# Optimization experiments

Hardware: AMD Instinct MI355X
Metric: run time of the kernel (lower is better)

Reference implementation:

```python
import jax, jax.numpy as jnp
import numpy as np

N, VQ, VK, C, H = 4, 4096, 4096, 128, 64


def setup_inputs() -> dict:
    key = jax.random.key(0)
    kx, ky, kq, kk, kv = jax.random.split(key, 5)
    # xavier-uniform-ish scale for params
    def xavier(k, shape):
        fan_in, fan_out = shape
        lim = (6.0 / (fan_in + fan_out)) ** 0.5
        return jax.random.uniform(k, shape, jnp.float32, -lim, lim)
    return {
        "x": jax.random.normal(kx, (N, VQ, C), jnp.float32),
        "y": jax.random.normal(ky, (N, VK, C), jnp.float32),
        "Wq": xavier(kq, (C, H)),
        "Wk": xavier(kk, (C, H)),
        "Wv": xavier(kv, (C, C)),
    }


def reference(x, y, Wq, Wk, Wv):
    # x: [n, vq, c], y: [n, vk, c]
    scale = Wq.shape[1] ** (-0.5)
    q = jnp.einsum('nvc,co->nvo', x, Wq)   # [n, vq, h]
    k = jnp.einsum('nvc,co->nvo', y, Wk)   # [n, vk, h]
    v = jnp.einsum('nvc,co->nvo', y, Wv)   # [n, vk, c]
    scores = jnp.einsum('nqc,nkc->nqk', q, k) * scale  # [n, vq, vk]
    attn = jax.nn.softmax(scores, axis=-1)
    return jnp.einsum('nqk,nkc->nqc', attn, v)         # [n, vq, c]
```

## Files before the change

kernel.cpp:

```cpp
#include <hip/hip_runtime.h>

typedef __bf16 bf16x8 __attribute__((ext_vector_type(8)));
typedef __bf16 bf16x4 __attribute__((ext_vector_type(4)));
typedef __bf16 bf16x2 __attribute__((ext_vector_type(2)));
typedef float  f32x4  __attribute__((ext_vector_type(4)));
typedef float  f32x16 __attribute__((ext_vector_type(16)));
typedef int    i32x4  __attribute__((ext_vector_type(4)));

#define MFMA16 __builtin_amdgcn_mfma_f32_16x16x32_bf16
#define MFMA32 __builtin_amdgcn_mfma_f32_32x32x16_bf16

static constexpr int BATCH = 4;
static constexpr int SEQ   = 4096;
static constexpr int CDIM  = 128;
static constexpr int HDIM  = 64;
static constexpr float FIXMAX = 16.0f;

union FB2  { bf16x2 h; int i; };
union I4B8 { i32x4 i; bf16x8 b; };

__device__ inline bf16x8 load8f_cvt(const float* __restrict__ p) {
    f32x4 a = *reinterpret_cast<const f32x4*>(p);
    f32x4 b = *reinterpret_cast<const f32x4*>(p + 4);
    bf16x8 r;
    r[0] = (__bf16)a[0]; r[1] = (__bf16)a[1]; r[2] = (__bf16)a[2]; r[3] = (__bf16)a[3];
    r[4] = (__bf16)b[0]; r[5] = (__bf16)b[1]; r[6] = (__bf16)b[2]; r[7] = (__bf16)b[3];
    return r;
}


__global__ __launch_bounds__(256) void proj_all_kernel(
    const float* __restrict__ x, const float* __restrict__ y,
    const float* __restrict__ Wq, const float* __restrict__ Wk,
    const float* __restrict__ Wv,
    __bf16* __restrict__ Qw, __bf16* __restrict__ Kw, __bf16* __restrict__ Vtw,
    float qscale)
{
    __shared__ __bf16 Wt[64][136];
    __shared__ __bf16 Vtile[64][72];

    const int job = blockIdx.x >> 8;
    const int bx  = blockIdx.x & 255;
    const int t    = threadIdx.x;
    const int lane = t & 63;
    const int w    = t >> 6;
    const int m    = lane & 15;
    const int quad = lane >> 4;

    if (job <= 1) {
        const float* X    = job ? y  : x;
        const float* W    = job ? Wk : Wq;
        __bf16*      outp = job ? Kw : Qw;
        const float scale = job ? 1.0f : qscale;

        #pragma unroll
        for (int pass = 0; pass < 4; ++pass) {
            int flat = pass * 2048 + t * 8;
            int cin  = flat >> 6;
            int h0   = flat & 63;
            bf16x8 v = load8f_cvt(W + flat);
            #pragma unroll
            for (int j = 0; j < 8; ++j) Wt[h0 + j][cin] = v[j];
        }
        __syncthreads();

        const int row0 = bx * 64 + w * 16;
        bf16x8 af[4];
        #pragma unroll
        for (int kc = 0; kc < 4; ++kc)
            af[kc] = load8f_cvt(X + (long)(row0 + m) * 128 + kc * 32 + quad * 8);

        #pragma unroll
        for (int tn = 0; tn < 4; ++tn) {
            f32x4 acc = {0.f, 0.f, 0.f, 0.f};
            #pragma unroll
            for (int kc = 0; kc < 4; ++kc) {
                bf16x8 bfrag = *reinterpret_cast<const bf16x8*>(&Wt[tn * 16 + m][kc * 32 + quad * 8]);
                acc = MFMA16(af[kc], bfrag, acc, 0, 0, 0);
            }
            #pragma unroll
            for (int r = 0; r < 4; ++r) {
                int  kg   = row0 + quad * 4 + r;
                long addr = ((long)(kg >> 5) * 4 + tn) * 512
                          + ((m >> 3) * 32 + (kg & 31)) * 8 + (m & 7);
                outp[addr] = (__bf16)(acc[r] * scale);
            }
        }
    } else {
        const int cob = (job - 2) * 64;
        const int ct0 = (job - 2) * 2;

        #pragma unroll
        for (int pass = 0; pass < 4; ++pass) {
            int flat = pass * 2048 + t * 8;
            int cin  = flat >> 6;
            int co0  = flat & 63;
            bf16x8 v = load8f_cvt(Wv + cin * 128 + cob + co0);
            #pragma unroll
            for (int j = 0; j < 8; ++j) Wt[co0 + j][cin] = v[j];
        }
        __syncthreads();

        const int row0 = bx * 64 + w * 16;
        bf16x8 af[4];
        #pragma unroll
        for (int kc = 0; kc < 4; ++kc)
            af[kc] = load8f_cvt(y + (long)(row0 + m) * 128 + kc * 32 + quad * 8);

        #pragma unroll
        for (int tn = 0; tn < 4; ++tn) {
            f32x4 acc = {0.f, 0.f, 0.f, 0.f};
            #pragma unroll
            for (int kc = 0; kc < 4; ++kc) {
                bf16x8 bfrag = *reinterpret_cast<const bf16x8*>(&Wt[tn * 16 + m][kc * 32 + quad * 8]);
                acc = MFMA16(af[kc], bfrag, acc, 0, 0, 0);
            }
            bf16x4 pk;
            #pragma unroll
            for (int r = 0; r < 4; ++r) pk[r] = (__bf16)acc[r];
            *reinterpret_cast<bf16x4*>(&Vtile[tn * 16 + m][w * 16 + quad * 4]) = pk;
        }
        __syncthreads();

        #pragma unroll
        for (int pp = 0; pp < 2; ++pp) {
            int i       = pp * 256 + t;
            int c_local = i & 31;
            int hh      = (i >> 5) & 1;
            int kc2     = (i >> 6) & 1;
            int ct_l    = (i >> 7) & 1;
            int kt_l    = i >> 8;
            bf16x8 v = *reinterpret_cast<const bf16x8*>(
                &Vtile[ct_l * 32 + c_local][kt_l * 32 + kc2 * 16 + hh * 8]);
            long dst = ((long)(bx * 2 + kt_l) * 8 + (ct0 + ct_l) * 2 + kc2) * 512
                     + (hh * 32 + c_local) * 8;
            *reinterpret_cast<bf16x8*>(Vtw + dst) = v;
        }
    }
}

__device__ __forceinline__ void attn_iter(
    const bf16x8 (&qf)[4],
    const bf16x8 (&kf)[4], bf16x8 (&kfn)[4],
    const bf16x8 (&vf)[8], bf16x8 (&vfn)[8],
    const __bf16* __restrict__ kp_next, const __bf16* __restrict__ vp_next,
    bool prefetch, f32x16 (&o_acc)[4],
    float& l_a, float& l_b, float& l_c, float& l_d)
{
    if (prefetch) {
        #pragma unroll
        for (int kc = 0; kc < 4; ++kc)
            kfn[kc] = *reinterpret_cast<const bf16x8*>(kp_next + kc * 512);
        #pragma unroll
        for (int c = 0; c < 8; ++c)
            vfn[c] = *reinterpret_cast<const bf16x8*>(vp_next + c * 512);
    }

    f32x16 s;
    #pragma unroll
    for (int i = 0; i < 16; ++i) s[i] = -FIXMAX;
    __builtin_amdgcn_s_setprio(1);
    #pragma unroll
    for (int kc = 0; kc < 4; ++kc)
        s = MFMA32(kf[kc], qf[kc], s, 0, 0, 0);
    __builtin_amdgcn_s_setprio(0);

    #pragma unroll
    for (int kc2 = 0; kc2 < 2; ++kc2) {
        float& lx = kc2 ? l_c : l_a;
        float& ly = kc2 ? l_d : l_b;
        int Dw[4];
        #pragma unroll
        for (int r2 = 0; r2 < 4; ++r2) {
            float p0 = __builtin_amdgcn_exp2f(s[8 * kc2 + 2 * r2]);
            float p1 = __builtin_amdgcn_exp2f(s[8 * kc2 + 2 * r2 + 1]);
            lx += p0; ly += p1;
            FB2 u; u.h[0] = (__bf16)p0; u.h[1] = (__bf16)p1;
            Dw[r2] = u.i;
        }
        int a0 = Dw[0], a1 = Dw[1], a2 = Dw[2], a3 = Dw[3];
        asm("v_permlane32_swap_b32 %0, %1" : "+v"(a0), "+v"(a2));
        asm("v_permlane32_swap_b32 %0, %1" : "+v"(a1), "+v"(a3));
        I4B8 pb;
        pb.i[0] = a0;
        pb.i[1] = a1;
        pb.i[2] = a2;
        pb.i[3] = a3;
        __builtin_amdgcn_s_setprio(1);
        #pragma unroll
        for (int ct = 0; ct < 4; ++ct)
            o_acc[ct] = MFMA32(vf[ct * 2 + kc2], pb.b, o_acc[ct], 0, 0, 0);
        __builtin_amdgcn_s_setprio(0);
    }
}

__global__ __launch_bounds__(512, 2) void attn_kernel(
    const __bf16* __restrict__ Qs, const __bf16* __restrict__ Ks,
    const __bf16* __restrict__ Vs, float* __restrict__ out)
{
    __shared__ float mbuf[2][2][64][65];

    const int t    = threadIdx.x;
    const int lane = t & 63;
    const int w    = t >> 6;
    const int qs   = w & 1;
    const int g    = w >> 1;
    const int qc   = lane & 31;
    const int h    = lane >> 5;

    const int bx  = blockIdx.x;
    const int n   = bx >> 6;
    const int qtl = bx & 63;

    const long QT = (long)n * 128 + qtl * 2 + qs;
    bf16x8 qf[4];
    #pragma unroll
    for (int kc = 0; kc < 4; ++kc)
        qf[kc] = *reinterpret_cast<const bf16x8*>(Qs + (QT * 4 + kc) * 512 + lane * 8);

    const __bf16* kb = Ks + ((long)n * 128 + g * 32) * 2048 + lane * 8;
    const __bf16* vb = Vs + ((long)n * 128 + g * 32) * 4096 + lane * 8;

    f32x16 o_acc[4];
    #pragma unroll
    for (int a = 0; a < 4; ++a)
        #pragma unroll
        for (int i = 0; i < 16; ++i) o_acc[a][i] = 0.f;
    float l_a = 0.f, l_b = 0.f, l_c = 0.f, l_d = 0.f;

    bf16x8 kf0[4], kf1[4];
    bf16x8 vf0[8], vf1[8];

    #pragma unroll
    for (int kc = 0; kc < 4; ++kc)
        kf0[kc] = *reinterpret_cast<const bf16x8*>(kb + kc * 512);
    #pragma unroll
    for (int c = 0; c < 8; ++c)
        vf0[c] = *reinterpret_cast<const bf16x8*>(vb + c * 512);

    for (int kt = 0; kt < 32; kt += 2) {
        attn_iter(qf, kf0, kf1, vf0, vf1,
                  kb + (long)(kt + 1) * 2048, vb + (long)(kt + 1) * 4096,
                  true, o_acc, l_a, l_b, l_c, l_d);
        attn_iter(qf, kf1, kf0, vf1, vf0,
                  kb + (long)(kt + 2) * 2048, vb + (long)(kt + 2) * 4096,
                  kt < 30, o_acc, l_a, l_b, l_c, l_d);
    }

    float l_run = (l_a + l_b) + (l_c + l_d);

    if (g >= 2) {
        float* dst = &mbuf[qs][g - 2][lane][0];
        #pragma unroll
        for (int ct = 0; ct < 4; ++ct)
            #pragma unroll
            for (int i = 0; i < 16; ++i) dst[ct * 16 + i] = o_acc[ct][i];
        dst[64] = l_run;
    }
    __syncthreads();
    if (g < 2) {
        const float* src = &mbuf[qs][g][lane][0];
        #pragma unroll
        for (int ct = 0; ct < 4; ++ct)
            #pragma unroll
            for (int i = 0; i < 16; ++i) o_acc[ct][i] += src[ct * 16 + i];
        l_run += src[64];
    }
    __syncthreads();
    if (g == 1) {
        float* dst = &mbuf[qs][0][lane][0];
        #pragma unroll
        for (int ct = 0; ct < 4; ++ct)
            #pragma unroll
            for (int i = 0; i < 16; ++i) dst[ct * 16 + i] = o_acc[ct][i];
        dst[64] = l_run;
    }
    __syncthreads();

    if (g == 0) {
        const float* src = &mbuf[qs][0][lane][0];
        #pragma unroll
        for (int ct = 0; ct < 4; ++ct)
            #pragma unroll
            for (int i = 0; i < 16; ++i) o_acc[ct][i] += src[ct * 16 + i];
        l_run += src[64];

        l_run += __shfl_xor(l_run, 32, 64);
        const float inv = 1.0f / l_run;
        const long row = (long)n * SEQ + qtl * 64 + qs * 32 + qc;
        #pragma unroll
        for (int ct = 0; ct < 4; ++ct)
            #pragma unroll
            for (int rg = 0; rg < 4; ++rg) {
                f32x4 o;
                #pragma unroll
                for (int i = 0; i < 4; ++i) o[i] = o_acc[ct][rg * 4 + i] * inv;
                *reinterpret_cast<f32x4*>(
                    out + row * CDIM + ct * 32 + rg * 8 + h * 4) = o;
            }
    }
}

extern "C" void kernel_launch(void* const* d_in, const int* in_sizes, int n_in,
                              void* d_out, int out_size, void* d_ws, size_t ws_size,
                              hipStream_t stream)
{
    const float* x  = (const float*)d_in[0];
    const float* y  = (const float*)d_in[1];
    const float* Wq = (const float*)d_in[2];
    const float* Wk = (const float*)d_in[3];
    const float* Wv = (const float*)d_in[4];
    float* out = (float*)d_out;

    __bf16* Qw  = (__bf16*)d_ws;
    __bf16* Kw  = Qw + (long)BATCH * SEQ * HDIM;
    __bf16* Vtw = Kw + (long)BATCH * SEQ * HDIM;

    const float qscale = 0.125f * 1.4426950408889634f;

    proj_all_kernel<<<dim3(1024), dim3(256), 0, stream>>>(
        x, y, Wq, Wk, Wv, Qw, Kw, Vtw, qscale);

    attn_kernel<<<dim3(256), dim3(512), 0, stream>>>(Qw, Kw, Vtw, out);
}
```

Baseline: 110.0 us.

## Split attention output channels across wave pairs and double the grid

Result: slower. 120.1 us (+9.2%).

```diff
diff --git a/kernel.cpp b/kernel.cpp
--- a/kernel.cpp
+++ b/kernel.cpp
@@ -139,164 +139,136 @@
     }
 }
 
-__device__ __forceinline__ void attn_iter(
-    const bf16x8 (&qf)[4],
-    const bf16x8 (&kf)[4], bf16x8 (&kfn)[4],
-    const bf16x8 (&vf)[8], bf16x8 (&vfn)[8],
-    const __bf16* __restrict__ kp_next, const __bf16* __restrict__ vp_next,
-    bool prefetch, f32x16 (&o_acc)[4],
-    float& l_a, float& l_b, float& l_c, float& l_d)
-{
-    if (prefetch) {
-        #pragma unroll
-        for (int kc = 0; kc < 4; ++kc)
-            kfn[kc] = *reinterpret_cast<const bf16x8*>(kp_next + kc * 512);
-        #pragma unroll
-        for (int c = 0; c < 8; ++c)
-            vfn[c] = *reinterpret_cast<const bf16x8*>(vp_next + c * 512);
-    }
-
-    f32x16 s;
-    #pragma unroll
-    for (int i = 0; i < 16; ++i) s[i] = -FIXMAX;
-    __builtin_amdgcn_s_setprio(1);
-    #pragma unroll
-    for (int kc = 0; kc < 4; ++kc)
-        s = MFMA32(kf[kc], qf[kc], s, 0, 0, 0);
-    __builtin_amdgcn_s_setprio(0);
-
-    #pragma unroll
-    for (int kc2 = 0; kc2 < 2; ++kc2) {
-        float& lx = kc2 ? l_c : l_a;
-        float& ly = kc2 ? l_d : l_b;
-        int Dw[4];
-        #pragma unroll
-        for (int r2 = 0; r2 < 4; ++r2) {
-            float p0 = __builtin_amdgcn_exp2f(s[8 * kc2 + 2 * r2]);
-            float p1 = __builtin_amdgcn_exp2f(s[8 * kc2 + 2 * r2 + 1]);
-            lx += p0; ly += p1;
-            FB2 u; u.h[0] = (__bf16)p0; u.h[1] = (__bf16)p1;
-            Dw[r2] = u.i;
-        }
-        int a0 = Dw[0], a1 = Dw[1], a2 = Dw[2], a3 = Dw[3];
-        asm("v_permlane32_swap_b32 %0, %1" : "+v"(a0), "+v"(a2));
-        asm("v_permlane32_swap_b32 %0, %1" : "+v"(a1), "+v"(a3));
-        I4B8 pb;
-        pb.i[0] = a0;
-        pb.i[1] = a1;
-        pb.i[2] = a2;
-        pb.i[3] = a3;
-        __builtin_amdgcn_s_setprio(1);
-        #pragma unroll
-        for (int ct = 0; ct < 4; ++ct)
-            o_acc[ct] = MFMA32(vf[ct * 2 + kc2], pb.b, o_acc[ct], 0, 0, 0);
-        __builtin_amdgcn_s_setprio(0);
-    }
-}
-
-__global__ __launch_bounds__(512, 2) void attn_kernel(
+__global__ __launch_bounds__(512, 4) void attn_kernel(
     const __bf16* __restrict__ Qs, const __bf16* __restrict__ Ks,
     const __bf16* __restrict__ Vs, float* __restrict__ out)
 {
-    __shared__ float mbuf[2][2][64][65];
+    __shared__ float mbuf[2][2][64][33];
 
     const int t    = threadIdx.x;
     const int lane = t & 63;
     const int w    = t >> 6;
-    const int qs   = w & 1;
+    const int ch   = w & 1;
     const int g    = w >> 1;
     const int qc   = lane & 31;
     const int h    = lane >> 5;
 
-    const int bx  = blockIdx.x;
-    const int n   = bx >> 6;
-    const int qtl = bx & 63;
-
-    const long QT = (long)n * 128 + qtl * 2 + qs;
+    const int bx   = blockIdx.x;
+    const int n    = bx >> 7;
+    const int qsub = bx & 127;
+
+    const long QT = (long)n * 128 + qsub;
     bf16x8 qf[4];
     #pragma unroll
     for (int kc = 0; kc < 4; ++kc)
         qf[kc] = *reinterpret_cast<const bf16x8*>(Qs + (QT * 4 + kc) * 512 + lane * 8);
 
     const __bf16* kb = Ks + ((long)n * 128 + g * 32) * 2048 + lane * 8;
-    const __bf16* vb = Vs + ((long)n * 128 + g * 32) * 4096 + lane * 8;
-
-    f32x16 o_acc[4];
+    const __bf16* vb = Vs + ((long)n * 128 + g * 32) * 4096 + ch * 2048 + lane * 8;
+
+    f32x16 o_acc[2];
     #pragma unroll
-    for (int a = 0; a < 4; ++a)
+    for (int a = 0; a < 2; ++a)
         #pragma unroll
         for (int i = 0; i < 16; ++i) o_acc[a][i] = 0.f;
     float l_a = 0.f, l_b = 0.f, l_c = 0.f, l_d = 0.f;
 
-    bf16x8 kf0[4], kf1[4];
-    bf16x8 vf0[8], vf1[8];
-
-    #pragma unroll
-    for (int kc = 0; kc < 4; ++kc)
-        kf0[kc] = *reinterpret_cast<const bf16x8*>(kb + kc * 512);
-    #pragma unroll
-    for (int c = 0; c < 8; ++c)
-        vf0[c] = *reinterpret_cast<const bf16x8*>(vb + c * 512);
-
-    for (int kt = 0; kt < 32; kt += 2) {
-        attn_iter(qf, kf0, kf1, vf0, vf1,
-                  kb + (long)(kt + 1) * 2048, vb + (long)(kt + 1) * 4096,
-                  true, o_acc, l_a, l_b, l_c, l_d);
-        attn_iter(qf, kf1, kf0, vf1, vf0,
-                  kb + (long)(kt + 2) * 2048, vb + (long)(kt + 2) * 4096,
-                  kt < 30, o_acc, l_a, l_b, l_c, l_d);
+    for (int kt = 0; kt < 32; ++kt) {
+        bf16x8 kf[4], vf[4];
+        #pragma unroll
+        for (int kc = 0; kc < 4; ++kc)
+            kf[kc] = *reinterpret_cast<const bf16x8*>(kb + ((long)kt * 4 + kc) * 512);
+        #pragma unroll
+        for (int c = 0; c < 4; ++c)
+            vf[c] = *reinterpret_cast<const bf16x8*>(vb + (long)kt * 4096 + c * 512);
+
+        f32x16 s;
+        #pragma unroll
+        for (int i = 0; i < 16; ++i) s[i] = -FIXMAX;
+        __builtin_amdgcn_s_setprio(1);
+        #pragma unroll
+        for (int kc = 0; kc < 4; ++kc)
+            s = MFMA32(kf[kc], qf[kc], s, 0, 0, 0);
+        __builtin_amdgcn_s_setprio(0);
+
+        #pragma unroll
+        for (int kc2 = 0; kc2 < 2; ++kc2) {
+            float& lx = kc2 ? l_c : l_a;
+            float& ly = kc2 ? l_d : l_b;
+            int Dw[4];
+            #pragma unroll
+            for (int r2 = 0; r2 < 4; ++r2) {
+                float p0 = __builtin_amdgcn_exp2f(s[8 * kc2 + 2 * r2]);
+                float p1 = __builtin_amdgcn_exp2f(s[8 * kc2 + 2 * r2 + 1]);
+                lx += p0; ly += p1;
+                FB2 u; u.h[0] = (__bf16)p0; u.h[1] = (__bf16)p1;
+                Dw[r2] = u.i;
+            }
+            int a0 = Dw[0], a1 = Dw[1], a2 = Dw[2], a3 = Dw[3];
+            asm("v_permlane32_swap_b32 %0, %1" : "+v"(a0), "+v"(a2));
+            asm("v_permlane32_swap_b32 %0, %1" : "+v"(a1), "+v"(a3));
+            I4B8 pb;
+            pb.i[0] = a0;
+            pb.i[1] = a1;
+            pb.i[2] = a2;
+            pb.i[3] = a3;
+            __builtin_amdgcn_s_setprio(1);
+            o_acc[0] = MFMA32(vf[kc2],     pb.b, o_acc[0], 0, 0, 0);
+            o_acc[1] = MFMA32(vf[2 + kc2], pb.b, o_acc[1], 0, 0, 0);
+            __builtin_amdgcn_s_setprio(0);
+        }
     }
 
     float l_run = (l_a + l_b) + (l_c + l_d);
 
     if (g >= 2) {
-        float* dst = &mbuf[qs][g - 2][lane][0];
-        #pragma unroll
-        for (int ct = 0; ct < 4; ++ct)
-            #pragma unroll
-            for (int i = 0; i < 16; ++i) dst[ct * 16 + i] = o_acc[ct][i];
-        dst[64] = l_run;
+        float* dst = &mbuf[ch][g - 2][lane][0];
+        #pragma unroll
+        for (int ctl = 0; ctl < 2; ++ctl)
+            #pragma unroll
+            for (int i = 0; i < 16; ++i) dst[ctl * 16 + i] = o_acc[ctl][i];
+        dst[32] = l_run;
     }
     __syncthreads();
     if (g < 2) {
-        const float* src = &mbuf[qs][g][lane][0];
-        #pragma unroll
-        for (int ct = 0; ct < 4; ++ct)
-            #pragma unroll
-            for (int i = 0; i < 16; ++i) o_acc[ct][i] += src[ct * 16 + i];
-        l_run += src[64];
+        const float* src = &mbuf[ch][g][lane][0];
+        #pragma unroll
+        for (int ctl = 0; ctl < 2; ++ctl)
+            #pragma unroll
+            for (int i = 0; i < 16; ++i) o_acc[ctl][i] += src[ctl * 16 + i];
+        l_run += src[32];
     }
     __syncthreads();
     if (g == 1) {
-        float* dst = &mbuf[qs][0][lane][0];
-        #pragma unroll
-        for (int ct = 0; ct < 4; ++ct)
-            #pragma unroll
-            for (int i = 0; i < 16; ++i) dst[ct * 16 + i] = o_acc[ct][i];
-        dst[64] = l_run;
+        float* dst = &mbuf[ch][0][lane][0];
+        #pragma unroll
+        for (int ctl = 0; ctl < 2; ++ctl)
+            #pragma unroll
+            for (int i = 0; i < 16; ++i) dst[ctl * 16 + i] = o_acc[ctl][i];
+        dst[32] = l_run;
     }
     __syncthreads();
 
     if (g == 0) {
-        const float* src = &mbuf[qs][0][lane][0];
-        #pragma unroll
-        for (int ct = 0; ct < 4; ++ct)
-            #pragma unroll
-            for (int i = 0; i < 16; ++i) o_acc[ct][i] += src[ct * 16 + i];
-        l_run += src[64];
+        const float* src = &mbuf[ch][0][lane][0];
+        #pragma unroll
+        for (int ctl = 0; ctl < 2; ++ctl)
+            #pragma unroll
+            for (int i = 0; i < 16; ++i) o_acc[ctl][i] += src[ctl * 16 + i];
+        l_run += src[32];
 
         l_run += __shfl_xor(l_run, 32, 64);
         const float inv = 1.0f / l_run;
-        const long row = (long)n * SEQ + qtl * 64 + qs * 32 + qc;
-        #pragma unroll
-        for (int ct = 0; ct < 4; ++ct)
+        const long row = (long)n * SEQ + qsub * 32 + qc;
+        #pragma unroll
+        for (int ctl = 0; ctl < 2; ++ctl)
             #pragma unroll
             for (int rg = 0; rg < 4; ++rg) {
                 f32x4 o;
                 #pragma unroll
-                for (int i = 0; i < 4; ++i) o[i] = o_acc[ct][rg * 4 + i] * inv;
+                for (int i = 0; i < 4; ++i) o[i] = o_acc[ctl][rg * 4 + i] * inv;
                 *reinterpret_cast<f32x4*>(
-                    out + row * CDIM + ct * 32 + rg * 8 + h * 4) = o;
+                    out + row * CDIM + ch * 64 + ctl * 32 + rg * 8 + h * 4) = o;
             }
     }
 }
@@ -321,5 +293,5 @@
     proj_all_kernel<<<dim3(1024), dim3(256), 0, stream>>>(
         x, y, Wq, Wk, Wv, Qw, Kw, Vtw, qscale);
 
-    attn_kernel<<<dim3(256), dim3(512), 0, stream>>>(Qw, Kw, Vtw, out);
-}
+    attn_kernel<<<dim3(512), dim3(512), 0, stream>>>(Qw, Kw, Vtw, out);
+}
```

## Split attention blocks to one query tile and drop V double-buffering

Applied to the files above, without the earlier changes.

New measurement: 177.5 us. 1.61x slower.

```diff
diff --git a/kernel.cpp b/kernel.cpp
--- a/kernel.cpp
+++ b/kernel.cpp
@@ -142,18 +142,18 @@
 __device__ __forceinline__ void attn_iter(
     const bf16x8 (&qf)[4],
     const bf16x8 (&kf)[4], bf16x8 (&kfn)[4],
-    const bf16x8 (&vf)[8], bf16x8 (&vfn)[8],
-    const __bf16* __restrict__ kp_next, const __bf16* __restrict__ vp_next,
-    bool prefetch, f32x16 (&o_acc)[4],
-    float& l_a, float& l_b, float& l_c, float& l_d)
+    const __bf16* __restrict__ vp,
+    const __bf16* __restrict__ kp_next,
+    bool prefetch, f32x16 (&o_acc)[4], float& l_a, float& l_b)
 {
+    bf16x8 vfA[4];
+    #pragma unroll
+    for (int ct = 0; ct < 4; ++ct)
+        vfA[ct] = *reinterpret_cast<const bf16x8*>(vp + (2 * ct) * 512);
     if (prefetch) {
         #pragma unroll
         for (int kc = 0; kc < 4; ++kc)
             kfn[kc] = *reinterpret_cast<const bf16x8*>(kp_next + kc * 512);
-        #pragma unroll
-        for (int c = 0; c < 8; ++c)
-            vfn[c] = *reinterpret_cast<const bf16x8*>(vp_next + c * 512);
     }
 
     f32x16 s;
@@ -165,16 +165,19 @@
         s = MFMA32(kf[kc], qf[kc], s, 0, 0, 0);
     __builtin_amdgcn_s_setprio(0);
 
+    bf16x8 vfB[4];
+    #pragma unroll
+    for (int ct = 0; ct < 4; ++ct)
+        vfB[ct] = *reinterpret_cast<const bf16x8*>(vp + (2 * ct + 1) * 512);
+
     #pragma unroll
     for (int kc2 = 0; kc2 < 2; ++kc2) {
-        float& lx = kc2 ? l_c : l_a;
-        float& ly = kc2 ? l_d : l_b;
         int Dw[4];
         #pragma unroll
         for (int r2 = 0; r2 < 4; ++r2) {
             float p0 = __builtin_amdgcn_exp2f(s[8 * kc2 + 2 * r2]);
             float p1 = __builtin_amdgcn_exp2f(s[8 * kc2 + 2 * r2 + 1]);
-            lx += p0; ly += p1;
+            l_a += p0; l_b += p1;
             FB2 u; u.h[0] = (__bf16)p0; u.h[1] = (__bf16)p1;
             Dw[r2] = u.i;
         }
@@ -189,30 +192,28 @@
         __builtin_amdgcn_s_setprio(1);
         #pragma unroll
         for (int ct = 0; ct < 4; ++ct)
-            o_acc[ct] = MFMA32(vf[ct * 2 + kc2], pb.b, o_acc[ct], 0, 0, 0);
+            o_acc[ct] = MFMA32(kc2 ? vfB[ct] : vfA[ct], pb.b, o_acc[ct], 0, 0, 0);
         __builtin_amdgcn_s_setprio(0);
     }
 }
 
-__global__ __launch_bounds__(512, 2) void attn_kernel(
+__global__ __launch_bounds__(256, 3) void attn_kernel(
     const __bf16* __restrict__ Qs, const __bf16* __restrict__ Ks,
     const __bf16* __restrict__ Vs, float* __restrict__ out)
 {
-    __shared__ float mbuf[2][2][64][65];
+    __shared__ float mbuf[2][64][65];
 
     const int t    = threadIdx.x;
     const int lane = t & 63;
-    const int w    = t >> 6;
-    const int qs   = w & 1;
-    const int g    = w >> 1;
+    const int g    = t >> 6;
     const int qc   = lane & 31;
     const int h    = lane >> 5;
 
-    const int bx  = blockIdx.x;
-    const int n   = bx >> 6;
-    const int qtl = bx & 63;
-
-    const long QT = (long)n * 128 + qtl * 2 + qs;
+    const int bx   = blockIdx.x;
+    const int n    = bx >> 7;
+    const int qsub = bx & 127;
+
+    const long QT = (long)n * 128 + qsub;
     bf16x8 qf[4];
     #pragma unroll
     for (int kc = 0; kc < 4; ++kc)
@@ -226,31 +227,27 @@
     for (int a = 0; a < 4; ++a)
         #pragma unroll
         for (int i = 0; i < 16; ++i) o_acc[a][i] = 0.f;
-    float l_a = 0.f, l_b = 0.f, l_c = 0.f, l_d = 0.f;
+    float l_a = 0.f, l_b = 0.f;
 
     bf16x8 kf0[4], kf1[4];
-    bf16x8 vf0[8], vf1[8];
 
     #pragma unroll
     for (int kc = 0; kc < 4; ++kc)
         kf0[kc] = *reinterpret_cast<const bf16x8*>(kb + kc * 512);
-    #pragma unroll
-    for (int c = 0; c < 8; ++c)
-        vf0[c] = *reinterpret_cast<const bf16x8*>(vb + c * 512);
 
     for (int kt = 0; kt < 32; kt += 2) {
-        attn_iter(qf, kf0, kf1, vf0, vf1,
-                  kb + (long)(kt + 1) * 2048, vb + (long)(kt + 1) * 4096,
-                  true, o_acc, l_a, l_b, l_c, l_d);
-        attn_iter(qf, kf1, kf0, vf1, vf0,
-                  kb + (long)(kt + 2) * 2048, vb + (long)(kt + 2) * 4096,
-                  kt < 30, o_acc, l_a, l_b, l_c, l_d);
-    }
-
-    float l_run = (l_a + l_b) + (l_c + l_d);
+        attn_iter(qf, kf0, kf1, vb + (long)kt * 4096,
+                  kb + (long)(kt + 1) * 2048,
+                  true, o_acc, l_a, l_b);
+        attn_iter(qf, kf1, kf0, vb + (long)(kt + 1) * 4096,
+                  kb + (long)(kt + 2) * 2048,
+                  kt < 30, o_acc, l_a, l_b);
+    }
+
+    float l_run = l_a + l_b;
 
     if (g >= 2) {
-        float* dst = &mbuf[qs][g - 2][lane][0];
+        float* dst = &mbuf[g - 2][lane][0];
         #pragma unroll
         for (int ct = 0; ct < 4; ++ct)
             #pragma unroll
@@ -259,7 +256,7 @@
     }
     __syncthreads();
     if (g < 2) {
-        const float* src = &mbuf[qs][g][lane][0];
+        const float* src = &mbuf[g][lane][0];
         #pragma unroll
         for (int ct = 0; ct < 4; ++ct)
             #pragma unroll
@@ -268,7 +265,7 @@
     }
     __syncthreads();
     if (g == 1) {
-        float* dst = &mbuf[qs][0][lane][0];
+        float* dst = &mbuf[0][lane][0];
         #pragma unroll
         for (int ct = 0; ct < 4; ++ct)
             #pragma unroll
@@ -278,7 +275,7 @@
     __syncthreads();
 
     if (g == 0) {
-        const float* src = &mbuf[qs][0][lane][0];
+        const float* src = &mbuf[0][lane][0];
         #pragma unroll
         for (int ct = 0; ct < 4; ++ct)
             #pragma unroll
@@ -287,7 +284,7 @@
 
         l_run += __shfl_xor(l_run, 32, 64);
         const float inv = 1.0f / l_run;
-        const long row = (long)n * SEQ + qtl * 64 + qs * 32 + qc;
+        const long row = (long)n * SEQ + qsub * 32 + qc;
         #pragma unroll
         for (int ct = 0; ct < 4; ++ct)
             #pragma unroll
@@ -321,5 +318,5 @@
     proj_all_kernel<<<dim3(1024), dim3(256), 0, stream>>>(
         x, y, Wq, Wk, Wv, Qw, Kw, Vtw, qscale);
 
-    attn_kernel<<<dim3(256), dim3(512), 0, stream>>>(Qw, Kw, Vtw, out);
-}
+    attn_kernel<<<dim3(512), dim3(256), 0, stream>>>(Qw, Kw, Vtw, out);
+}
```

## Software-pipeline QK^T one tile ahead of softmax and PV in attention loop

Applied to the files above, without the earlier changes.

Measured after the change: 110.2 us. About the same (+0.2%).

```diff
diff --git a/kernel.cpp b/kernel.cpp
--- a/kernel.cpp
+++ b/kernel.cpp
@@ -141,29 +141,36 @@
 
 __device__ __forceinline__ void attn_iter(
     const bf16x8 (&qf)[4],
-    const bf16x8 (&kf)[4], bf16x8 (&kfn)[4],
-    const bf16x8 (&vf)[8], bf16x8 (&vfn)[8],
-    const __bf16* __restrict__ kp_next, const __bf16* __restrict__ vp_next,
-    bool prefetch, f32x16 (&o_acc)[4],
+    const bf16x8 (&kfq)[4],
+    bf16x8 (&kfp)[4],
+    const bf16x8 (&vf)[8],
+    bf16x8 (&vfp)[8],
+    const __bf16* __restrict__ kp2, const __bf16* __restrict__ vp1,
+    bool pref_k, bool pref_v, bool do_qk,
+    f32x16& s_cur, f32x16& s_next,
+    f32x16 (&o_acc)[4],
     float& l_a, float& l_b, float& l_c, float& l_d)
 {
-    if (prefetch) {
+    if (pref_k) {
         #pragma unroll
         for (int kc = 0; kc < 4; ++kc)
-            kfn[kc] = *reinterpret_cast<const bf16x8*>(kp_next + kc * 512);
+            kfp[kc] = *reinterpret_cast<const bf16x8*>(kp2 + kc * 512);
+    }
+    if (pref_v) {
         #pragma unroll
         for (int c = 0; c < 8; ++c)
-            vfn[c] = *reinterpret_cast<const bf16x8*>(vp_next + c * 512);
-    }
-
-    f32x16 s;
-    #pragma unroll
-    for (int i = 0; i < 16; ++i) s[i] = -FIXMAX;
-    __builtin_amdgcn_s_setprio(1);
-    #pragma unroll
-    for (int kc = 0; kc < 4; ++kc)
-        s = MFMA32(kf[kc], qf[kc], s, 0, 0, 0);
-    __builtin_amdgcn_s_setprio(0);
+            vfp[c] = *reinterpret_cast<const bf16x8*>(vp1 + c * 512);
+    }
+
+    if (do_qk) {
+        #pragma unroll
+        for (int i = 0; i < 16; ++i) s_next[i] = -FIXMAX;
+        __builtin_amdgcn_s_setprio(1);
+        #pragma unroll
+        for (int kc = 0; kc < 4; ++kc)
+            s_next = MFMA32(kfq[kc], qf[kc], s_next, 0, 0, 0);
+        __builtin_amdgcn_s_setprio(0);
+    }
 
     #pragma unroll
     for (int kc2 = 0; kc2 < 2; ++kc2) {
@@ -172,8 +179,8 @@
         int Dw[4];
         #pragma unroll
         for (int r2 = 0; r2 < 4; ++r2) {
-            float p0 = __builtin_amdgcn_exp2f(s[8 * kc2 + 2 * r2]);
-            float p1 = __builtin_amdgcn_exp2f(s[8 * kc2 + 2 * r2 + 1]);
+            float p0 = __builtin_amdgcn_exp2f(s_cur[8 * kc2 + 2 * r2]);
+            float p1 = __builtin_amdgcn_exp2f(s_cur[8 * kc2 + 2 * r2 + 1]);
             lx += p0; ly += p1;
             FB2 u; u.h[0] = (__bf16)p0; u.h[1] = (__bf16)p1;
             Dw[r2] = u.i;
@@ -230,21 +237,32 @@
 
     bf16x8 kf0[4], kf1[4];
     bf16x8 vf0[8], vf1[8];
+    f32x16 s_a, s_b;
 
     #pragma unroll
     for (int kc = 0; kc < 4; ++kc)
         kf0[kc] = *reinterpret_cast<const bf16x8*>(kb + kc * 512);
     #pragma unroll
+    for (int i = 0; i < 16; ++i) s_a[i] = -FIXMAX;
+    #pragma unroll
+    for (int kc = 0; kc < 4; ++kc)
+        s_a = MFMA32(kf0[kc], qf[kc], s_a, 0, 0, 0);
+    #pragma unroll
+    for (int kc = 0; kc < 4; ++kc)
+        kf1[kc] = *reinterpret_cast<const bf16x8*>(kb + 2048 + kc * 512);
+    #pragma unroll
     for (int c = 0; c < 8; ++c)
         vf0[c] = *reinterpret_cast<const bf16x8*>(vb + c * 512);
 
     for (int kt = 0; kt < 32; kt += 2) {
-        attn_iter(qf, kf0, kf1, vf0, vf1,
-                  kb + (long)(kt + 1) * 2048, vb + (long)(kt + 1) * 4096,
-                  true, o_acc, l_a, l_b, l_c, l_d);
-        attn_iter(qf, kf1, kf0, vf1, vf0,
-                  kb + (long)(kt + 2) * 2048, vb + (long)(kt + 2) * 4096,
-                  kt < 30, o_acc, l_a, l_b, l_c, l_d);
+        attn_iter(qf, kf1, kf0, vf0, vf1,
+                  kb + (long)(kt + 2) * 2048, vb + (long)(kt + 1) * 4096,
+                  kt < 30, true, true,
+                  s_a, s_b, o_acc, l_a, l_b, l_c, l_d);
+        attn_iter(qf, kf0, kf1, vf1, vf0,
+                  kb + (long)(kt + 3) * 2048, vb + (long)(kt + 2) * 4096,
+                  kt < 30, kt < 30, kt < 30,
+                  s_b, s_a, o_acc, l_a, l_b, l_c, l_d);
     }
 
     float l_run = (l_a + l_b) + (l_c + l_d);
```
